# Performance work log

Hardware: AMD Instinct MI355X
Metric: run time of the kernel (lower is better)

Reference implementation:

```python
import jax, jax.numpy as jnp
import numpy as np

NUM_TREES = 256
DEPTH = 6
TREE_DIM = 2
INPUT_DIM = 256
BATCH = 2048


def sparsemax(x, axis=0):
    # Euclidean projection onto the simplex along `axis`.
    x = jnp.moveaxis(x, axis, -1)
    z = jnp.flip(jnp.sort(x, axis=-1), axis=-1)           # descending
    cz = jnp.cumsum(z, axis=-1)
    k = jnp.arange(1, x.shape[-1] + 1, dtype=x.dtype)
    support = (1.0 + k * z) > cz                          # boolean support set
    k_sel = jnp.sum(support, axis=-1, keepdims=True)      # |S(z)|
    tau = (jnp.take_along_axis(cz, k_sel - 1, axis=-1) - 1.0) / k_sel.astype(x.dtype)
    out = jnp.maximum(x - tau, 0.0)
    return jnp.moveaxis(out, -1, axis)


def sparsemoid(x):
    return jnp.clip(0.5 * x + 0.5, 0.0, 1.0)


def make_bin_codes(depth):
    idx = np.arange(2 ** depth)
    offs = 2 ** np.arange(depth)
    bc = ((idx[None, :] // offs[:, None]) % 2).astype(np.float32)  # [depth, 2^depth]
    return jnp.asarray(np.stack([bc, 1.0 - bc], axis=-1))          # [depth, 2^depth, 2]


def setup_inputs() -> dict:
    key = jax.random.key(0)
    ks = jax.random.split(key, 5)
    return {
        "inputs": jax.random.normal(ks[0], (BATCH, INPUT_DIM), dtype=jnp.float32),
        "feature_selection_logits": jax.random.normal(ks[1], (INPUT_DIM, NUM_TREES, DEPTH), dtype=jnp.float32),
        "feature_thresholds": jax.random.normal(ks[2], (NUM_TREES, DEPTH), dtype=jnp.float32) * 0.5,
        "log_temperatures": jax.random.normal(ks[3], (NUM_TREES, DEPTH), dtype=jnp.float32) * 0.1,
        "response": jax.random.normal(ks[4], (NUM_TREES, TREE_DIM, 2 ** DEPTH), dtype=jnp.float32),
    }


def reference(inputs, feature_selection_logits, feature_thresholds, log_temperatures, response):
    bin_codes_1hot = make_bin_codes(DEPTH)                                  # [d, 2^d, 2]
    selectors = sparsemax(feature_selection_logits, axis=0)                 # [i, n, d]
    feature_values = jnp.einsum('bi,ind->bnd', inputs, selectors)           # [b, n, d]
    tl = (feature_values - feature_thresholds) * jnp.exp(-log_temperatures) # [b, n, d]
    threshold_logits = jnp.stack([-tl, tl], axis=-1)                        # [b, n, d, 2]
    bins = sparsemoid(threshold_logits)                                     # [b, n, d, 2]
    bin_matches = jnp.einsum('bnds,dcs->bndc', bins, bin_codes_1hot)        # [b, n, d, 2^d]
    response_weights = jnp.prod(bin_matches, axis=-2)                       # [b, n, 2^d]
    out = jnp.einsum('bnc,ntc->bnt', response_weights, response)            # [b, n, tree_dim]
    return out.reshape(out.shape[0], -1)                                    # [b, n*tree_dim]
```

## Files before the change

### kernel.cpp

```cpp
#include <hip/hip_runtime.h>
#include <hip/hip_fp16.h>
#include <math.h>

#define NUM_TREES 256
#define DEPTH 6
#define TREE_DIM 2
#define INPUT_DIM 256
#define BATCH 2048
#define NLEAF 64
#define NCOLS (NUM_TREES * DEPTH)
#define KDIM INPUT_DIM

typedef _Float16 half8 __attribute__((ext_vector_type(8)));
typedef float floatx4 __attribute__((ext_vector_type(4)));

__global__ __launch_bounds__(256) void sparsemax_bisect(
    const float* __restrict__ fsl,
    _Float16* __restrict__ selT)
{
    const int lane = threadIdx.x & 63;
    const int wave = threadIdx.x >> 6;
    const int col  = blockIdx.x * 4 + wave;
    const int n = col / 6;
    const int d = col - n * 6;

    float x[4];
#pragma unroll
    for (int j = 0; j < 4; ++j)
        x[j] = fsl[(j * 64 + lane) * NCOLS + col];

    float mx = fmaxf(fmaxf(x[0], x[1]), fmaxf(x[2], x[3]));
#pragma unroll
    for (int off = 32; off > 0; off >>= 1)
        mx = fmaxf(mx, __shfl_xor(mx, off));

    float lo = mx - 1.0f, hi = mx;
    for (int it = 0; it < 24; ++it) {
        const float mid = 0.5f * (lo + hi);
        float s = fmaxf(x[0] - mid, 0.0f) + fmaxf(x[1] - mid, 0.0f)
                + fmaxf(x[2] - mid, 0.0f) + fmaxf(x[3] - mid, 0.0f);
#pragma unroll
        for (int off = 32; off > 0; off >>= 1)
            s += __shfl_xor(s, off);
        if (s > 1.0f) lo = mid; else hi = mid;
    }
    const float tau = 0.5f * (lo + hi);

    _Float16* dst = selT + (n * 8 + d) * KDIM;
#pragma unroll
    for (int j = 0; j < 4; ++j)
        dst[j * 64 + lane] = (_Float16)fmaxf(x[j] - tau, 0.0f);
}

#define BM 128
#define BN 64
#define BK 32
#define FVS 68

__global__ __launch_bounds__(256) void odt_mfma_kernel(
    const float* __restrict__ inputs,
    const _Float16* __restrict__ selT,
    const float* __restrict__ thr,
    const float* __restrict__ logt,
    const float* __restrict__ resp,
    float* __restrict__ out)
{
    __shared__ _Float16 Asm[BM][BK];
    __shared__ _Float16 Bsm[BN][BK];
    __shared__ float    fvS[BM][FVS];
    __shared__ float    respS[8 * TREE_DIM * NLEAF];

    const int tid = threadIdx.x;
    const int b0 = blockIdx.x * BM;
    const int treeBase = blockIdx.y * 8;
    const int colBase  = blockIdx.y * BN;

    ((float4*)respS)[tid] = ((const float4*)(resp + treeBase * TREE_DIM * NLEAF))[tid];

    const int lane = tid & 63;
    const int w    = tid >> 6;
    const int wm   = w >> 1, wn = w & 1;
    const int l16  = lane & 15, quad = lane >> 4;

    floatx4 acc[4][2];
#pragma unroll
    for (int mt = 0; mt < 4; ++mt)
#pragma unroll
        for (int nt = 0; nt < 2; ++nt)
            acc[mt][nt] = (floatx4){0.f, 0.f, 0.f, 0.f};

    const int arow = tid >> 1, ach = tid & 1;
    const int bcol = tid >> 2, bkc = tid & 3;

    for (int k0 = 0; k0 < KDIM; k0 += BK) {
        __syncthreads();
        {
            const float4* g = (const float4*)(inputs + (b0 + arow) * KDIM + k0 + ach * 16);
            const float4 v0 = g[0], v1 = g[1], v2 = g[2], v3 = g[3];
            half8 h0, h1;
            h0[0] = (_Float16)v0.x; h0[1] = (_Float16)v0.y; h0[2] = (_Float16)v0.z; h0[3] = (_Float16)v0.w;
            h0[4] = (_Float16)v1.x; h0[5] = (_Float16)v1.y; h0[6] = (_Float16)v1.z; h0[7] = (_Float16)v1.w;
            h1[0] = (_Float16)v2.x; h1[1] = (_Float16)v2.y; h1[2] = (_Float16)v2.z; h1[3] = (_Float16)v2.w;
            h1[4] = (_Float16)v3.x; h1[5] = (_Float16)v3.y; h1[6] = (_Float16)v3.z; h1[7] = (_Float16)v3.w;
            *(half8*)&Asm[arow][ach * 16]     = h0;
            *(half8*)&Asm[arow][ach * 16 + 8] = h1;
        }
        {
            const half8 v = *(const half8*)(selT + (colBase + bcol) * KDIM + k0 + bkc * 8);
            *(half8*)&Bsm[bcol][bkc * 8] = v;
        }
        __syncthreads();

        half8 bfr0 = *(half8*)&Bsm[wn * 32 + l16][quad * 8];
        half8 bfr1 = *(half8*)&Bsm[wn * 32 + 16 + l16][quad * 8];
#pragma unroll
        for (int mt = 0; mt < 4; ++mt) {
            half8 afr = *(half8*)&Asm[wm * 64 + mt * 16 + l16][quad * 8];
            acc[mt][0] = __builtin_amdgcn_mfma_f32_16x16x32_f16(afr, bfr0, acc[mt][0], 0, 0, 0);
            acc[mt][1] = __builtin_amdgcn_mfma_f32_16x16x32_f16(afr, bfr1, acc[mt][1], 0, 0, 0);
        }
    }

#pragma unroll
    for (int mt = 0; mt < 4; ++mt)
#pragma unroll
        for (int nt = 0; nt < 2; ++nt)
#pragma unroll
            for (int r = 0; r < 4; ++r)
                fvS[wm * 64 + mt * 16 + quad * 4 + r][wn * 32 + nt * 16 + l16] = acc[mt][nt][r];
    __syncthreads();

#pragma unroll
    for (int p = 0; p < 4; ++p) {
        const int idx = tid + 256 * p;
        const int row = idx & 127;
        const int tl  = idx >> 7;
        const int n   = treeBase + tl;
        const float* f = &fvS[row][tl * 8];

        float sd[DEPTH];
#pragma unroll
        for (int d = 0; d < DEPTH; ++d) {
            const float tlg = (f[d] - thr[n * DEPTH + d]) * __expf(-logt[n * DEPTH + d]);
            sd[d] = fminf(fmaxf(0.5f + 0.5f * tlg, 0.0f), 1.0f);
        }
        float wv[NLEAF];
        wv[0] = 1.0f;
#pragma unroll
        for (int d = 0; d < DEPTH; ++d) {
            const int sz = 1 << d;
#pragma unroll
            for (int c2 = 0; c2 < NLEAF / 2; ++c2) {
                if (c2 < sz) {
                    const float t = wv[c2];
                    wv[c2]      = t * sd[d];
                    wv[c2 + sz] = t * (1.0f - sd[d]);
                }
            }
        }
        const float* r0 = &respS[tl * TREE_DIM * NLEAF];
        float o0 = 0.0f, o1 = 0.0f;
#pragma unroll
        for (int c2 = 0; c2 < NLEAF; ++c2) {
            o0 = fmaf(wv[c2], r0[c2], o0);
            o1 = fmaf(wv[c2], r0[NLEAF + c2], o1);
        }
        float2 o = {o0, o1};
        *(float2*)(out + (b0 + row) * (NUM_TREES * TREE_DIM) + n * TREE_DIM) = o;
    }
}

extern "C" void kernel_launch(void* const* d_in, const int* in_sizes, int n_in,
                              void* d_out, int out_size, void* d_ws, size_t ws_size,
                              hipStream_t stream) {
    const float* inputs = (const float*)d_in[0];
    const float* fsl    = (const float*)d_in[1];
    const float* thr    = (const float*)d_in[2];
    const float* logt   = (const float*)d_in[3];
    const float* resp   = (const float*)d_in[4];
    float* out = (float*)d_out;
    _Float16* selT = (_Float16*)d_ws;

    hipLaunchKernelGGL(sparsemax_bisect, dim3(NCOLS / 4), dim3(256), 0, stream, fsl, selT);
    hipLaunchKernelGGL(odt_mfma_kernel, dim3(BATCH / BM, (NUM_TREES * 8) / BN), dim3(256),
                       0, stream, inputs, selT, thr, logt, resp, out);
}
```

Measured before the change: 91.08 us.

## Pre-convert inputs to fp16 in prologue kernel, widen BK, share LDS via union

The first kernel now also converts the fp32 inputs to fp16 into workspace, so the GEMM kernel loads half-precision A tiles instead of re-converting fp32 in every block. BK is doubled to 64 with padded LDS rows, halving the number of k-iterations and barriers. The A/B tiles are unioned with the feature-value staging buffer to cut LDS footprint. Bisection iterations drop from 24 to 16, which is cheaper but less precise in tau (about 1.5e-5 interval width).

After: 91.81 us. No clear change (+0.8%).

```diff
diff --git a/kernel.cpp b/kernel.cpp
--- a/kernel.cpp
+++ b/kernel.cpp
@@ -16,10 +16,27 @@
 
 __global__ __launch_bounds__(256) void sparsemax_bisect(
     const float* __restrict__ fsl,
-    _Float16* __restrict__ selT)
+    const float* __restrict__ inputs,
+    _Float16* __restrict__ selT,
+    _Float16* __restrict__ inH)
 {
-    const int lane = threadIdx.x & 63;
-    const int wave = threadIdx.x >> 6;
+    const int tid = threadIdx.x;
+    {
+        const int gid = blockIdx.x * 256 + tid;
+        if (gid < (BATCH * INPUT_DIM) / 8) {
+            const float4 v0 = ((const float4*)inputs)[gid * 2];
+            const float4 v1 = ((const float4*)inputs)[gid * 2 + 1];
+            half8 h;
+            h[0] = (_Float16)v0.x; h[1] = (_Float16)v0.y;
+            h[2] = (_Float16)v0.z; h[3] = (_Float16)v0.w;
+            h[4] = (_Float16)v1.x; h[5] = (_Float16)v1.y;
+            h[6] = (_Float16)v1.z; h[7] = (_Float16)v1.w;
+            *(half8*)(inH + gid * 8) = h;
+        }
+    }
+
+    const int lane = tid & 63;
+    const int wave = tid >> 6;
     const int col  = blockIdx.x * 4 + wave;
     const int n = col / 6;
     const int d = col - n * 6;
@@ -35,7 +52,7 @@
         mx = fmaxf(mx, __shfl_xor(mx, off));
 
     float lo = mx - 1.0f, hi = mx;
-    for (int it = 0; it < 24; ++it) {
+    for (int it = 0; it < 16; ++it) {
         const float mid = 0.5f * (lo + hi);
         float s = fmaxf(x[0] - mid, 0.0f) + fmaxf(x[1] - mid, 0.0f)
                 + fmaxf(x[2] - mid, 0.0f) + fmaxf(x[3] - mid, 0.0f);
@@ -54,21 +71,27 @@
 
 #define BM 128
 #define BN 64
-#define BK 32
+#define BK 64
+#define AP 72
+#define BP 72
 #define FVS 68
 
 __global__ __launch_bounds__(256) void odt_mfma_kernel(
-    const float* __restrict__ inputs,
+    const _Float16* __restrict__ inH,
     const _Float16* __restrict__ selT,
     const float* __restrict__ thr,
     const float* __restrict__ logt,
     const float* __restrict__ resp,
     float* __restrict__ out)
 {
-    __shared__ _Float16 Asm[BM][BK];
-    __shared__ _Float16 Bsm[BN][BK];
-    __shared__ float    fvS[BM][FVS];
-    __shared__ float    respS[8 * TREE_DIM * NLEAF];
+    __shared__ union {
+        struct {
+            _Float16 A[BM][AP];
+            _Float16 B[BN][BP];
+        } s;
+        float fv[BM][FVS];
+    } u;
+    __shared__ float respS[8 * TREE_DIM * NLEAF];
 
     const int tid = threadIdx.x;
     const int b0 = blockIdx.x * BM;
@@ -89,37 +112,45 @@
         for (int nt = 0; nt < 2; ++nt)
             acc[mt][nt] = (floatx4){0.f, 0.f, 0.f, 0.f};
 
-    const int arow = tid >> 1, ach = tid & 1;
-    const int bcol = tid >> 2, bkc = tid & 3;
+    const int arow = tid >> 1, ahr = tid & 1;
+    const int bcol = tid >> 2, bq  = tid & 3;
 
     for (int k0 = 0; k0 < KDIM; k0 += BK) {
         __syncthreads();
         {
-            const float4* g = (const float4*)(inputs + (b0 + arow) * KDIM + k0 + ach * 16);
-            const float4 v0 = g[0], v1 = g[1], v2 = g[2], v3 = g[3];
-            half8 h0, h1;
-            h0[0] = (_Float16)v0.x; h0[1] = (_Float16)v0.y; h0[2] = (_Float16)v0.z; h0[3] = (_Float16)v0.w;
-            h0[4] = (_Float16)v1.x; h0[5] = (_Float16)v1.y; h0[6] = (_Float16)v1.z; h0[7] = (_Float16)v1.w;
-            h1[0] = (_Float16)v2.x; h1[1] = (_Float16)v2.y; h1[2] = (_Float16)v2.z; h1[3] = (_Float16)v2.w;
-            h1[4] = (_Float16)v3.x; h1[5] = (_Float16)v3.y; h1[6] = (_Float16)v3.z; h1[7] = (_Float16)v3.w;
-            *(half8*)&Asm[arow][ach * 16]     = h0;
-            *(half8*)&Asm[arow][ach * 16 + 8] = h1;
+            const _Float16* ag = inH + (b0 + arow) * KDIM + k0 + ahr * 32;
+            const half8 a0 = *(const half8*)(ag);
+            const half8 a1 = *(const half8*)(ag + 8);
+            const half8 a2 = *(const half8*)(ag + 16);
+            const half8 a3 = *(const half8*)(ag + 24);
+            *(half8*)&u.s.A[arow][ahr * 32 + 0]  = a0;
+            *(half8*)&u.s.A[arow][ahr * 32 + 8]  = a1;
+            *(half8*)&u.s.A[arow][ahr * 32 + 16] = a2;
+            *(half8*)&u.s.A[arow][ahr * 32 + 24] = a3;
         }
         {
-            const half8 v = *(const half8*)(selT + (colBase + bcol) * KDIM + k0 + bkc * 8);
-            *(half8*)&Bsm[bcol][bkc * 8] = v;
+            const _Float16* bg = selT + (colBase + bcol) * KDIM + k0 + bq * 16;
+            const half8 b0v = *(const half8*)(bg);
+            const half8 b1v = *(const half8*)(bg + 8);
+            *(half8*)&u.s.B[bcol][bq * 16 + 0] = b0v;
+            *(half8*)&u.s.B[bcol][bq * 16 + 8] = b1v;
         }
         __syncthreads();
 
-        half8 bfr0 = *(half8*)&Bsm[wn * 32 + l16][quad * 8];
-        half8 bfr1 = *(half8*)&Bsm[wn * 32 + 16 + l16][quad * 8];
-#pragma unroll
-        for (int mt = 0; mt < 4; ++mt) {
-            half8 afr = *(half8*)&Asm[wm * 64 + mt * 16 + l16][quad * 8];
-            acc[mt][0] = __builtin_amdgcn_mfma_f32_16x16x32_f16(afr, bfr0, acc[mt][0], 0, 0, 0);
-            acc[mt][1] = __builtin_amdgcn_mfma_f32_16x16x32_f16(afr, bfr1, acc[mt][1], 0, 0, 0);
-        }
-    }
+#pragma unroll
+        for (int h = 0; h < 2; ++h) {
+            const half8 bf0 = *(const half8*)&u.s.B[wn * 32 + l16][quad * 8 + h * 32];
+            const half8 bf1 = *(const half8*)&u.s.B[wn * 32 + 16 + l16][quad * 8 + h * 32];
+#pragma unroll
+            for (int mt = 0; mt < 4; ++mt) {
+                const half8 af = *(const half8*)&u.s.A[wm * 64 + mt * 16 + l16][quad * 8 + h * 32];
+                acc[mt][0] = __builtin_amdgcn_mfma_f32_16x16x32_f16(af, bf0, acc[mt][0], 0, 0, 0);
+                acc[mt][1] = __builtin_amdgcn_mfma_f32_16x16x32_f16(af, bf1, acc[mt][1], 0, 0, 0);
+            }
+        }
+    }
+
+    __syncthreads();
 
 #pragma unroll
     for (int mt = 0; mt < 4; ++mt)
@@ -127,7 +158,7 @@
         for (int nt = 0; nt < 2; ++nt)
 #pragma unroll
             for (int r = 0; r < 4; ++r)
-                fvS[wm * 64 + mt * 16 + quad * 4 + r][wn * 32 + nt * 16 + l16] = acc[mt][nt][r];
+                u.fv[wm * 64 + mt * 16 + quad * 4 + r][wn * 32 + nt * 16 + l16] = acc[mt][nt][r];
     __syncthreads();
 
 #pragma unroll
@@ -136,7 +167,7 @@
         const int row = idx & 127;
         const int tl  = idx >> 7;
         const int n   = treeBase + tl;
-        const float* f = &fvS[row][tl * 8];
+        const float* f = &u.fv[row][tl * 8];
 
         float sd[DEPTH];
 #pragma unroll
@@ -180,8 +211,10 @@
     const float* resp   = (const float*)d_in[4];
     float* out = (float*)d_out;
     _Float16* selT = (_Float16*)d_ws;
-
-    hipLaunchKernelGGL(sparsemax_bisect, dim3(NCOLS / 4), dim3(256), 0, stream, fsl, selT);
-    hipLaunchKernelGGL(odt_mfma_kernel, dim3(BATCH / BM, (NUM_TREES * 8) / BN), dim3(256),
-                       0, stream, inputs, selT, thr, logt, resp, out);
+    _Float16* inH  = (_Float16*)((char*)d_ws + (1 << 20));
+
+    hipLaunchKernelGGL(sparsemax_bisect, dim3(NCOLS / 4), dim3(256), 0, stream,
+                       fsl, inputs, selT, inH);
+    hipLaunchKernelGGL(odt_mfma_kernel, dim3(BATCH / BM, NUM_TREES / 8), dim3(256),
+                       0, stream, inH, selT, thr, logt, resp, out);
 }
```
